# Performance work log

Measured on AMD Instinct MI355X. Metric: run time of the kernel, lower is better.

Reference implementation:

```python
import jax, jax.numpy as jnp
import numpy as np

STRIDE = 8
PAD = 8
KSZ = 16


def setup_inputs() -> dict:
    key = jax.random.key(0)
    k1, k2, k3 = jax.random.split(key, 3)
    B, Cin, Cout, L = 16, 512, 1, 4000
    inp = jax.random.normal(k1, (B, Cin, L), dtype=jnp.float32)
    # t60 in [0.1, 0.5) so that round(t60*100)-10 lands in [0, 40]
    t60s = 0.1 + 0.39 * jax.random.uniform(k2, (B // 2,), dtype=jnp.float32)
    kernel_weight = jax.random.uniform(k3, (41, Cin, Cout, KSZ), dtype=jnp.float32)
    return {"input": inp, "t60s": t60s, "kernel_weight": kernel_weight}


def reference(input, t60s, kernel_weight):
    # per-sample kernel index: round(t60*100).int().repeat(2) - 10
    idx = jnp.tile(jnp.round(t60s * 100.0).astype(jnp.int32), 2) - 10  # (B,)
    w = kernel_weight[idx]                      # (B, Cin, Cout, K) gathered per sample
    # torch conv_transpose1d(x, W) == conv(x with lhs_dilation=stride,
    #                                      flip_k(W).swap(Cin,Cout), pad=K-1-p)
    w = jnp.flip(jnp.swapaxes(w, 1, 2), axis=-1)  # (B, Cout, Cin, K)
    pad = KSZ - 1 - PAD

    def per_sample(x, wk):  # x: (Cin, L), wk: (Cout, Cin, K)
        y = jax.lax.conv_general_dilated(
            x[None], wk,
            window_strides=(1,),
            padding=[(pad, pad)],
            lhs_dilation=(STRIDE,),
            dimension_numbers=("NCH", "OIH", "NCH"),
        )
        return y[0]  # (Cout, L_out), L_out = (L-1)*stride - 2*PAD + K

    return jax.vmap(per_sample)(input, w)  # (B, Cout, L_out)
```

## Files before the change

### kernel.cpp

```cpp
#include <hip/hip_runtime.h>

#define L_IN    4000
#define CIN     512
#define KSZ     16
#define LOUT    31992
#define NQ      3999
#define QPB     256
#define RSTRIDE 2304

__global__ __launch_bounds__(512, 2)
void dereverb_kernel(const float* __restrict__ x,
                     const float* __restrict__ t60s,
                     const float* __restrict__ kw,
                     float* __restrict__ out)
{
    __shared__ float lds[8 * RSTRIDE];

    const int b    = blockIdx.y;
    const int q0   = blockIdx.x * QPB;
    const int tid  = threadIdx.x;
    const int lane = tid & 63;
    const int wave = tid >> 6;

    float t60 = t60s[b & 7];
    int kidx = (int)rintf(t60 * 100.0f) - 10;
    kidx = __builtin_amdgcn_readfirstlane(kidx);
    const float4* wsrc = (const float4*)(kw + (size_t)kidx * (CIN * KSZ));

    #pragma unroll
    for (int i = 0; i < 4; ++i)
        ((float4*)lds)[tid + i * 512] = wsrc[tid + i * 512];
    __syncthreads();

    const float* xb = x + ((size_t)b * CIN + wave * 64) * L_IN;
    const float* xp[4];
    #pragma unroll
    for (int qi = 0; qi < 4; ++qi) {
        int q  = q0 + qi * 64 + lane;
        int qc = q < NQ - 1 ? q : (NQ - 1);
        xp[qi] = xb + qc;
    }

    const float4* wl = (const float4*)(lds + wave * 64 * KSZ);

    float acc[4][8];
    #pragma unroll
    for (int qi = 0; qi < 4; ++qi)
        #pragma unroll
        for (int r = 0; r < 8; ++r) acc[qi][r] = 0.0f;

    #pragma unroll 2
    for (int ci = 0; ci < 64; ++ci) {
        float x0[4], x1[4];
        #pragma unroll
        for (int qi = 0; qi < 4; ++qi) {
            x0[qi] = xp[qi][0];
            x1[qi] = xp[qi][1];
            xp[qi] += L_IN;
        }
        float4 wv[4];
        wv[0] = wl[0];
        wv[1] = wl[1];
        wv[2] = wl[2];
        wv[3] = wl[3];
        wl += 4;
        const float* wf = (const float*)wv;
        #pragma unroll
        for (int qi = 0; qi < 4; ++qi)
            #pragma unroll
            for (int r = 0; r < 8; ++r) {
                acc[qi][r] = fmaf(x1[qi], wf[r],     acc[qi][r]);
                acc[qi][r] = fmaf(x0[qi], wf[r + 8], acc[qi][r]);
            }
    }

    #pragma unroll
    for (int qi = 0; qi < 4; ++qi)
        if (q0 + qi * 64 + lane > NQ - 1)
            #pragma unroll
            for (int r = 0; r < 8; ++r) acc[qi][r] = 0.0f;

    __syncthreads();
    #pragma unroll
    for (int qi = 0; qi < 4; ++qi) {
        int ql = qi * 64 + lane;
        float* rp = lds + wave * RSTRIDE + 9 * ql;
        #pragma unroll
        for (int r = 0; r < 8; ++r) rp[r] = acc[qi][r];
    }
    __syncthreads();

    const size_t ob = (size_t)b * LOUT + (size_t)q0 * 8;
    #pragma unroll
    for (int k = 0; k < 4; ++k) {
        int tl = k * 512 + tid;
        if (q0 * 8 + tl < LOUT) {
            int ql = tl >> 3, r = tl & 7;
            float s = 0.0f;
            #pragma unroll
            for (int w = 0; w < 8; ++w)
                s += lds[w * RSTRIDE + 9 * ql + r];
            out[ob + tl] = s;
        }
    }
}

extern "C" void kernel_launch(void* const* d_in, const int* in_sizes, int n_in,
                              void* d_out, int out_size, void* d_ws, size_t ws_size,
                              hipStream_t stream) {
    const float* x    = (const float*)d_in[0];
    const float* t60s = (const float*)d_in[1];
    const float* kw   = (const float*)d_in[2];
    float* out = (float*)d_out;

    dim3 grid((NQ + QPB - 1) / QPB, 16);
    dereverb_kernel<<<grid, 512, 0, stream>>>(x, t60s, kw, out);
}
```

Baseline: 190.9 us.

## Split channel reduction across 16 waves with two-pass LDS reduction

Doubles the block to 1024 threads so each wave reduces over 32 input channels instead of 64. The cross-wave reduction now runs in two passes over a halved LDS buffer: the upper 8 waves store their partials, the lower 8 add theirs, and all threads then sum 8 rows. The goal is more latency hiding and parallelism per block, since the grid has only 256 blocks. In exchange it adds extra barriers and LDS traffic, and occupancy limits may change with the 1024-thread launch bounds.

```diff
diff --git a/kernel.cpp b/kernel.cpp
--- a/kernel.cpp
+++ b/kernel.cpp
@@ -1,20 +1,20 @@
 #include <hip/hip_runtime.h>
 
-#define L_IN    4000
-#define CIN     512
-#define KSZ     16
-#define LOUT    31992
-#define NQ      3999
-#define QPB     256
-#define RSTRIDE 2304
+#define L_IN   4000
+#define CIN    512
+#define KSZ    16
+#define LOUT   31992
+#define NQ     3999
+#define QPB    256
+#define RST    1152
 
-__global__ __launch_bounds__(512, 2)
+__global__ __launch_bounds__(1024, 4)
 void dereverb_kernel(const float* __restrict__ x,
                      const float* __restrict__ t60s,
                      const float* __restrict__ kw,
                      float* __restrict__ out)
 {
-    __shared__ float lds[8 * RSTRIDE];
+    __shared__ float lds[8 * RST];
 
     const int b    = blockIdx.y;
     const int q0   = blockIdx.x * QPB;
@@ -27,12 +27,11 @@
     kidx = __builtin_amdgcn_readfirstlane(kidx);
     const float4* wsrc = (const float4*)(kw + (size_t)kidx * (CIN * KSZ));
 
-    #pragma unroll
-    for (int i = 0; i < 4; ++i)
-        ((float4*)lds)[tid + i * 512] = wsrc[tid + i * 512];
+    ((float4*)lds)[tid]        = wsrc[tid];
+    ((float4*)lds)[tid + 1024] = wsrc[tid + 1024];
     __syncthreads();
 
-    const float* xb = x + ((size_t)b * CIN + wave * 64) * L_IN;
+    const float* xb = x + ((size_t)b * CIN + wave * 32) * L_IN;
     const float* xp[4];
     #pragma unroll
     for (int qi = 0; qi < 4; ++qi) {
@@ -41,7 +40,7 @@
         xp[qi] = xb + qc;
     }
 
-    const float4* wl = (const float4*)(lds + wave * 64 * KSZ);
+    const float4* wl = (const float4*)(lds + wave * 32 * KSZ);
 
     float acc[4][8];
     #pragma unroll
@@ -49,8 +48,8 @@
         #pragma unroll
         for (int r = 0; r < 8; ++r) acc[qi][r] = 0.0f;
 
-    #pragma unroll 2
-    for (int ci = 0; ci < 64; ++ci) {
+    #pragma unroll 4
+    for (int ci = 0; ci < 32; ++ci) {
         float x0[4], x1[4];
         #pragma unroll
         for (int qi = 0; qi < 4; ++qi) {
@@ -80,27 +79,36 @@
             #pragma unroll
             for (int r = 0; r < 8; ++r) acc[qi][r] = 0.0f;
 
-    __syncthreads();
+    const size_t obase = (size_t)b * LOUT + (size_t)q0 * 8;
     #pragma unroll
-    for (int qi = 0; qi < 4; ++qi) {
-        int ql = qi * 64 + lane;
-        float* rp = lds + wave * RSTRIDE + 9 * ql;
-        #pragma unroll
-        for (int r = 0; r < 8; ++r) rp[r] = acc[qi][r];
-    }
-    __syncthreads();
-
-    const size_t ob = (size_t)b * LOUT + (size_t)q0 * 8;
-    #pragma unroll
-    for (int k = 0; k < 4; ++k) {
-        int tl = k * 512 + tid;
+    for (int p = 0; p < 2; ++p) {
+        __syncthreads();
+        if (wave >= 8) {
+            #pragma unroll
+            for (int h = 0; h < 2; ++h) {
+                float* rp = lds + (wave - 8) * RST + 9 * (h * 64 + lane);
+                #pragma unroll
+                for (int r = 0; r < 8; ++r) rp[r] = acc[2 * p + h][r];
+            }
+        }
+        __syncthreads();
+        if (wave < 8) {
+            #pragma unroll
+            for (int h = 0; h < 2; ++h) {
+                float* rp = lds + wave * RST + 9 * (h * 64 + lane);
+                #pragma unroll
+                for (int r = 0; r < 8; ++r) rp[r] += acc[2 * p + h][r];
+            }
+        }
+        __syncthreads();
+        int tl = p * 1024 + tid;
         if (q0 * 8 + tl < LOUT) {
-            int ql = tl >> 3, r = tl & 7;
+            int ql = tid >> 3, r = tid & 7;
             float s = 0.0f;
             #pragma unroll
             for (int w = 0; w < 8; ++w)
-                s += lds[w * RSTRIDE + 9 * ql + r];
-            out[ob + tl] = s;
+                s += lds[w * RST + 9 * ql + r];
+            out[obase + tl] = s;
         }
     }
 }
@@ -114,5 +122,5 @@
     float* out = (float*)d_out;
 
     dim3 grid((NQ + QPB - 1) / QPB, 16);
-    dereverb_kernel<<<grid, 512, 0, stream>>>(x, t60s, kw, out);
+    dereverb_kernel<<<grid, 1024, 0, stream>>>(x, t60s, kw, out);
 }
```

After: 195.6 us. 2.4% more time.
